# Kernel tuning notes

Hardware: AMD Instinct MI355X
Metric: run time of the kernel (lower is better)

The kernel has to match this reference:

```python
import jax, jax.numpy as jnp
import numpy as np

TOPK = 2
ROUTED_SCALING_FACTOR = 1.0


def setup_inputs() -> dict:
    key = jax.random.key(0)
    k1, k2 = jax.random.split(key)
    N, D, E = 8192, 4096, 64
    x = jax.random.normal(k1, (N, D), dtype=jnp.float32)
    expert_embeddings = jax.random.normal(k2, (E, D), dtype=jnp.float32) * 0.02
    gate_bias = jnp.zeros((E,), dtype=jnp.float32)
    return {"x": x, "expert_embeddings": expert_embeddings, "gate_bias": gate_bias}


def reference(x, expert_embeddings, gate_bias):
    # logits: (N, E) = x @ W^T, computed in fp32 as in the original
    logits = jnp.einsum('nd,ed->ne', x.astype(jnp.float32), expert_embeddings.astype(jnp.float32))
    scores = jax.nn.sigmoid(logits)
    biased_scores = scores + gate_bias  # bias only affects expert selection
    _, indices = jax.lax.top_k(biased_scores, TOPK)  # (N, topk)
    weights = jnp.take_along_axis(scores, indices, axis=-1)  # gather unbiased scores
    weights = weights / jnp.sum(weights, axis=-1, keepdims=True)
    weights = weights * ROUTED_SCALING_FACTOR
    return weights, indices, scores
```

## Files before the change

kernel.cpp:

```cpp
#include <hip/hip_runtime.h>
#include <hip/hip_bf16.h>
#include <math.h>

#define NROWS 8192
#define DDIM  4096
#define NEXP  64
#define KSPLIT 16
#define KCHUNK (DDIM / KSPLIT)
#define KSTEPS (KCHUNK / 32)

typedef __attribute__((ext_vector_type(8))) short bf16x8;
typedef __attribute__((ext_vector_type(4))) float f32x4;

__device__ inline unsigned short bf16_rne(float f) {
    unsigned u = __builtin_bit_cast(unsigned, f);
    u += 0x7FFF + ((u >> 16) & 1);
    return (unsigned short)(u >> 16);
}

__device__ inline void split8(const float* xf, bf16x8& hi, bf16x8& lo) {
#pragma unroll
    for (int j = 0; j < 8; j++) {
        const unsigned short h = bf16_rne(xf[j]);
        const float hf = __builtin_bit_cast(float, (unsigned)h << 16);
        hi[j] = (short)h;
        lo[j] = (short)bf16_rne(xf[j] - hf);
    }
}

__global__ __launch_bounds__(256) void wfrag_kernel(
    const float* __restrict__ w, unsigned short* __restrict__ whi,
    unsigned short* __restrict__ wlo, float* __restrict__ logits)
{
    const int kc = blockIdx.x;
    const int t  = threadIdx.x >> 6;
    const int l  = threadIdx.x & 63;
    const int e  = t * 16 + (l & 15);
    const int k0 = kc * 32 + ((l >> 4) * 8);
    const float* p = w + (size_t)e * DDIM + k0;
    float xf[8];
    *(float4*)&xf[0] = *(const float4*)p;
    *(float4*)&xf[4] = *(const float4*)(p + 4);
    bf16x8 hi, lo;
    split8(xf, hi, lo);
    const size_t off = ((size_t)(kc * 4 + t) * 64 + l) * 8;
    *(bf16x8*)(whi + off) = hi;
    *(bf16x8*)(wlo + off) = lo;

    const float4 z = {0.f, 0.f, 0.f, 0.f};
    float4* lz = (float4*)logits;
    const int base = (blockIdx.x * 256 + threadIdx.x) * 4;
#pragma unroll
    for (int j = 0; j < 4; j++) lz[base + j] = z;
}

__global__ __launch_bounds__(256) void gemm_partial_kernel(
    const float* __restrict__ x, const unsigned short* __restrict__ whi,
    const unsigned short* __restrict__ wlo, float* __restrict__ logits)
{
    __shared__ float ldsx[4 * 2 * 1024];

    const int tid = threadIdx.x;
    const int wv  = tid >> 6;
    const int l   = tid & 63;
    const int q   = l >> 4;
    const int col = l & 15;
    const int c7  = col & 7;
    const int r0  = blockIdx.x * 128 + wv * 32;
    const int kb  = blockIdx.y * KCHUNK;

    const int slr   = l >> 3;
    const int slotp = l & 7;

    float* ldsw = ldsx + wv * 2048;

    const unsigned short* bhp = whi + ((size_t)(kb / 32) * 4 * 64 + l) * 8;
    const unsigned short* blp = wlo + ((size_t)(kb / 32) * 4 * 64 + l) * 8;

    f32x4 acc[2][4];
#pragma unroll
    for (int m = 0; m < 2; m++)
#pragma unroll
        for (int t = 0; t < 4; t++) acc[m][t] = f32x4{0, 0, 0, 0};

    auto STAGE = [&](int buf, int s) {
#pragma unroll
        for (int g = 0; g < 4; g++) {
            const int lr   = g * 8 + slr;
            const int slot = slotp ^ (lr & 7);
            const float* gp = x + (size_t)(r0 + lr) * DDIM + kb + s * 32 + slot * 4;
            __builtin_amdgcn_global_load_lds(
                (const __attribute__((address_space(1))) void*)gp,
                (__attribute__((address_space(3))) void*)(ldsw + buf * 1024 + g * 256),
                16, 0, 0);
        }
    };

    STAGE(0, 0);
    __builtin_amdgcn_sched_barrier(0);

    for (int s = 0; s < KSTEPS; s++) {
        const int buf = s & 1;

        bf16x8 bh[4], bl[4];
        const unsigned short* bhs = bhp + (size_t)s * 4 * 64 * 8;
        const unsigned short* bls = blp + (size_t)s * 4 * 64 * 8;
#pragma unroll
        for (int t = 0; t < 4; t++) {
            bh[t] = *(const bf16x8*)(bhs + (size_t)t * 64 * 8);
            bl[t] = *(const bf16x8*)(bls + (size_t)t * 64 * 8);
        }

        asm volatile("s_waitcnt vmcnt(8)" ::: "memory");
        __builtin_amdgcn_sched_barrier(0);

        float xr[2][8];
#pragma unroll
        for (int m = 0; m < 2; m++) {
            const float* rb = ldsw + buf * 1024 + (m * 16 + col) * 32;
            const int sp0 = (q * 2) ^ c7;
            *(float4*)&xr[m][0] = *(const float4*)(rb + sp0 * 4);
            *(float4*)&xr[m][4] = *(const float4*)(rb + (sp0 ^ 1) * 4);
        }

        STAGE(buf ^ 1, (s + 1) & 7);
        __builtin_amdgcn_sched_barrier(0);

        bf16x8 ah[2], al[2];
        split8(xr[0], ah[0], al[0]);
        split8(xr[1], ah[1], al[1]);
#pragma unroll
        for (int m = 0; m < 2; m++)
#pragma unroll
            for (int t = 0; t < 4; t++) {
                acc[m][t] = __builtin_amdgcn_mfma_f32_16x16x32_bf16(ah[m], bh[t], acc[m][t], 0, 0, 0);
                acc[m][t] = __builtin_amdgcn_mfma_f32_16x16x32_bf16(ah[m], bl[t], acc[m][t], 0, 0, 0);
                acc[m][t] = __builtin_amdgcn_mfma_f32_16x16x32_bf16(al[m], bh[t], acc[m][t], 0, 0, 0);
            }
    }

#pragma unroll
    for (int m = 0; m < 2; m++)
#pragma unroll
        for (int t = 0; t < 4; t++)
#pragma unroll
            for (int r = 0; r < 4; r++)
                unsafeAtomicAdd(
                    &logits[(size_t)(r0 + m * 16 + q * 4 + r) * NEXP + t * 16 + col],
                    acc[m][t][r]);
}

__global__ __launch_bounds__(256) void gate_topk_kernel(
    const float* __restrict__ logits, const float* __restrict__ bias,
    float* __restrict__ out)
{
    const int tid = threadIdx.x;
    const int e   = tid & 63;
    const int row = blockIdx.x * 4 + (tid >> 6);
    const size_t idx = (size_t)row * NEXP + e;

    const float be    = bias[e];
    const float logit = logits[idx];
    const float score = 1.0f / (1.0f + expf(-logit));
    out[(size_t)4 * NROWS + idx] = score;

    const float biased = score + be;

    float v = biased; int bi = e;
#pragma unroll
    for (int off = 32; off; off >>= 1) {
        const float ov = __shfl_xor(v, off);
        const int   oi = __shfl_xor(bi, off);
        if (ov > v || (ov == v && oi < bi)) { v = ov; bi = oi; }
    }
    const int i1 = bi;

    float v2 = (e == i1) ? -INFINITY : biased;
    int bi2 = e;
#pragma unroll
    for (int off = 32; off; off >>= 1) {
        const float ov = __shfl_xor(v2, off);
        const int   oi = __shfl_xor(bi2, off);
        if (ov > v2 || (ov == v2 && oi < bi2)) { v2 = ov; bi2 = oi; }
    }
    const int i2 = bi2;

    const float s1 = __shfl(score, i1);
    const float s2 = __shfl(score, i2);
    if (e == 0) {
        const float inv = 1.0f / (s1 + s2);
        out[(size_t)row * 2 + 0] = s1 * inv;
        out[(size_t)row * 2 + 1] = s2 * inv;
        out[(size_t)2 * NROWS + row * 2 + 0] = (float)i1;
        out[(size_t)2 * NROWS + row * 2 + 1] = (float)i2;
    }
}

extern "C" void kernel_launch(void* const* d_in, const int* in_sizes, int n_in,
                              void* d_out, int out_size, void* d_ws, size_t ws_size,
                              hipStream_t stream)
{
    const float* x    = (const float*)d_in[0];
    const float* w    = (const float*)d_in[1];
    const float* bias = (const float*)d_in[2];
    float* out  = (float*)d_out;

    float* logits = (float*)d_ws;
    const size_t logits_bytes = (size_t)NROWS * NEXP * 4;
    unsigned short* whi = (unsigned short*)((char*)d_ws + logits_bytes);
    unsigned short* wlo = whi + (size_t)NEXP * DDIM;

    wfrag_kernel<<<DDIM / 32, 256, 0, stream>>>(w, whi, wlo, logits);
    dim3 g1(NROWS / 128, KSPLIT);
    gemm_partial_kernel<<<g1, 256, 0, stream>>>(x, whi, wlo, logits);
    gate_topk_kernel<<<NROWS / 4, 256, 0, stream>>>(logits, bias, out);
}
```

Baseline: 213.7 us.

## Triple-buffer x tiles in LDS and double-buffer W fragments in registers

Changes the split-K GEMM main loop from a two-slot LDS pipeline to a three-slot ring for the x tiles, with the async loads issued three steps ahead. The bf16 hi/lo W fragments are now loaded one step ahead into a register double buffer. Waitcnt values are adjusted to the new load order, and the loop is fully unrolled. The aim is to hide more global-load latency in this latency-bound loop, at the cost of 50% more LDS per block and more registers, which may lower occupancy.

After: 220.9 us. 1.03x slower.

```diff
diff --git a/kernel.cpp b/kernel.cpp
--- a/kernel.cpp
+++ b/kernel.cpp
@@ -58,7 +58,7 @@
     const float* __restrict__ x, const unsigned short* __restrict__ whi,
     const unsigned short* __restrict__ wlo, float* __restrict__ logits)
 {
-    __shared__ float ldsx[4 * 2 * 1024];
+    __shared__ float ldsx[4 * 3 * 1024];
 
     const int tid = threadIdx.x;
     const int wv  = tid >> 6;
@@ -72,7 +72,7 @@
     const int slr   = l >> 3;
     const int slotp = l & 7;
 
-    float* ldsw = ldsx + wv * 2048;
+    float* ldsw = ldsx + wv * 3072;
 
     const unsigned short* bhp = whi + ((size_t)(kb / 32) * 4 * 64 + l) * 8;
     const unsigned short* blp = wlo + ((size_t)(kb / 32) * 4 * 64 + l) * 8;
@@ -83,7 +83,9 @@
 #pragma unroll
         for (int t = 0; t < 4; t++) acc[m][t] = f32x4{0, 0, 0, 0};
 
-    auto STAGE = [&](int buf, int s) {
+    bf16x8 bh[2][4], bl[2][4];
+
+    auto STAGE = [&](int bufi, int s) {
 #pragma unroll
         for (int g = 0; g < 4; g++) {
             const int lr   = g * 8 + slr;
@@ -91,51 +93,61 @@
             const float* gp = x + (size_t)(r0 + lr) * DDIM + kb + s * 32 + slot * 4;
             __builtin_amdgcn_global_load_lds(
                 (const __attribute__((address_space(1))) void*)gp,
-                (__attribute__((address_space(3))) void*)(ldsw + buf * 1024 + g * 256),
+                (__attribute__((address_space(3))) void*)(ldsw + bufi * 1024 + g * 256),
                 16, 0, 0);
         }
     };
 
-    STAGE(0, 0);
-    __builtin_amdgcn_sched_barrier(0);
-
-    for (int s = 0; s < KSTEPS; s++) {
-        const int buf = s & 1;
-
-        bf16x8 bh[4], bl[4];
+    auto LOADB = [&](int rb, int s) {
         const unsigned short* bhs = bhp + (size_t)s * 4 * 64 * 8;
         const unsigned short* bls = blp + (size_t)s * 4 * 64 * 8;
 #pragma unroll
         for (int t = 0; t < 4; t++) {
-            bh[t] = *(const bf16x8*)(bhs + (size_t)t * 64 * 8);
-            bl[t] = *(const bf16x8*)(bls + (size_t)t * 64 * 8);
+            bh[rb][t] = *(const bf16x8*)(bhs + (size_t)t * 64 * 8);
+            bl[rb][t] = *(const bf16x8*)(bls + (size_t)t * 64 * 8);
         }
-
-        asm volatile("s_waitcnt vmcnt(8)" ::: "memory");
+    };
+
+    LOADB(0, 0);
+    STAGE(0, 0);
+    STAGE(1, 1);
+    STAGE(2, 2);
+    __builtin_amdgcn_sched_barrier(0);
+
+#pragma unroll
+    for (int s = 0; s < KSTEPS; s++) {
+        const int rb = s & 1;
+
+        if (s == 0) asm volatile("s_waitcnt vmcnt(8)" ::: "memory");
+        else        asm volatile("s_waitcnt vmcnt(4)" ::: "memory");
         __builtin_amdgcn_sched_barrier(0);
 
+        LOADB(rb ^ 1, (s + 1) & 7);
+        __builtin_amdgcn_sched_barrier(0);
+
         float xr[2][8];
 #pragma unroll
         for (int m = 0; m < 2; m++) {
-            const float* rb = ldsw + buf * 1024 + (m * 16 + col) * 32;
+            const float* rbp = ldsw + (s % 3) * 1024 + (m * 16 + col) * 32;
             const int sp0 = (q * 2) ^ c7;
-            *(float4*)&xr[m][0] = *(const float4*)(rb + sp0 * 4);
-            *(float4*)&xr[m][4] = *(const float4*)(rb + (sp0 ^ 1) * 4);
+            *(float4*)&xr[m][0] = *(const float4*)(rbp + sp0 * 4);
+            *(float4*)&xr[m][4] = *(const float4*)(rbp + (sp0 ^ 1) * 4);
         }
-
-        STAGE(buf ^ 1, (s + 1) & 7);
-        __builtin_amdgcn_sched_barrier(0);
 
         bf16x8 ah[2], al[2];
         split8(xr[0], ah[0], al[0]);
         split8(xr[1], ah[1], al[1]);
+
+        STAGE(s % 3, (s + 3) & 7);
+        __builtin_amdgcn_sched_barrier(0);
+
 #pragma unroll
         for (int m = 0; m < 2; m++)
 #pragma unroll
             for (int t = 0; t < 4; t++) {
-                acc[m][t] = __builtin_amdgcn_mfma_f32_16x16x32_bf16(ah[m], bh[t], acc[m][t], 0, 0, 0);
-                acc[m][t] = __builtin_amdgcn_mfma_f32_16x16x32_bf16(ah[m], bl[t], acc[m][t], 0, 0, 0);
-                acc[m][t] = __builtin_amdgcn_mfma_f32_16x16x32_bf16(al[m], bh[t], acc[m][t], 0, 0, 0);
+                acc[m][t] = __builtin_amdgcn_mfma_f32_16x16x32_bf16(ah[m], bh[rb][t], acc[m][t], 0, 0, 0);
+                acc[m][t] = __builtin_amdgcn_mfma_f32_16x16x32_bf16(ah[m], bl[rb][t], acc[m][t], 0, 0, 0);
+                acc[m][t] = __builtin_amdgcn_mfma_f32_16x16x32_bf16(al[m], bh[rb][t], acc[m][t], 0, 0, 0);
             }
     }
 
```

## Split K across waves in block and reduce partials in LDS instead of atomics

Applied to the files above, without the earlier changes.

Each block now covers 32 rows, and its four waves each take a different 256-wide K slice, so waves in a block share rows rather than rows being split across waves. Partial results are summed in LDS, and each of the four K-split blocks writes its own partial buffer. This replaces global float atomics and the zero-init of logits with plain stores. The top-k kernel then sums the four partials per logit. The costs are an extra LDS reduction with a __syncthreads, more workspace for the partial buffers, and four reads per logit in the gating kernel.

After: 211.8 us. No clear change (-0.9%).

```diff
diff --git a/kernel.cpp b/kernel.cpp
--- a/kernel.cpp
+++ b/kernel.cpp
@@ -5,9 +5,9 @@
 #define NROWS 8192
 #define DDIM  4096
 #define NEXP  64
-#define KSPLIT 16
+#define KSPLIT 4
 #define KCHUNK (DDIM / KSPLIT)
-#define KSTEPS (KCHUNK / 32)
+#define KSTEPS 8
 
 typedef __attribute__((ext_vector_type(8))) short bf16x8;
 typedef __attribute__((ext_vector_type(4))) float f32x4;
@@ -30,7 +30,7 @@
 
 __global__ __launch_bounds__(256) void wfrag_kernel(
     const float* __restrict__ w, unsigned short* __restrict__ whi,
-    unsigned short* __restrict__ wlo, float* __restrict__ logits)
+    unsigned short* __restrict__ wlo)
 {
     const int kc = blockIdx.x;
     const int t  = threadIdx.x >> 6;
@@ -46,17 +46,11 @@
     const size_t off = ((size_t)(kc * 4 + t) * 64 + l) * 8;
     *(bf16x8*)(whi + off) = hi;
     *(bf16x8*)(wlo + off) = lo;
-
-    const float4 z = {0.f, 0.f, 0.f, 0.f};
-    float4* lz = (float4*)logits;
-    const int base = (blockIdx.x * 256 + threadIdx.x) * 4;
-#pragma unroll
-    for (int j = 0; j < 4; j++) lz[base + j] = z;
 }
 
 __global__ __launch_bounds__(256) void gemm_partial_kernel(
     const float* __restrict__ x, const unsigned short* __restrict__ whi,
-    const unsigned short* __restrict__ wlo, float* __restrict__ logits)
+    const unsigned short* __restrict__ wlo, float* __restrict__ part)
 {
     __shared__ float ldsx[4 * 2 * 1024];
 
@@ -66,8 +60,9 @@
     const int q   = l >> 4;
     const int col = l & 15;
     const int c7  = col & 7;
-    const int r0  = blockIdx.x * 128 + wv * 32;
-    const int kb  = blockIdx.y * KCHUNK;
+    const int r0  = blockIdx.x * 32;
+    const int kh  = blockIdx.y;
+    const int kb  = kh * KCHUNK + wv * 256;
 
     const int slr   = l >> 3;
     const int slotp = l & 7;
@@ -99,6 +94,7 @@
     STAGE(0, 0);
     __builtin_amdgcn_sched_barrier(0);
 
+#pragma unroll
     for (int s = 0; s < KSTEPS; s++) {
         const int buf = s & 1;
 
@@ -117,13 +113,13 @@
         float xr[2][8];
 #pragma unroll
         for (int m = 0; m < 2; m++) {
-            const float* rb = ldsw + buf * 1024 + (m * 16 + col) * 32;
+            const float* rbp = ldsw + buf * 1024 + (m * 16 + col) * 32;
             const int sp0 = (q * 2) ^ c7;
-            *(float4*)&xr[m][0] = *(const float4*)(rb + sp0 * 4);
-            *(float4*)&xr[m][4] = *(const float4*)(rb + (sp0 ^ 1) * 4);
+            *(float4*)&xr[m][0] = *(const float4*)(rbp + sp0 * 4);
+            *(float4*)&xr[m][4] = *(const float4*)(rbp + (sp0 ^ 1) * 4);
         }
 
-        STAGE(buf ^ 1, (s + 1) & 7);
+        if (s + 1 < KSTEPS) STAGE(buf ^ 1, s + 1);
         __builtin_amdgcn_sched_barrier(0);
 
         bf16x8 ah[2], al[2];
@@ -139,19 +135,29 @@
             }
     }
 
+    asm volatile("s_waitcnt vmcnt(0)" ::: "memory");
+    __builtin_amdgcn_sched_barrier(0);
+
 #pragma unroll
     for (int m = 0; m < 2; m++)
 #pragma unroll
         for (int t = 0; t < 4; t++)
 #pragma unroll
             for (int r = 0; r < 4; r++)
-                unsafeAtomicAdd(
-                    &logits[(size_t)(r0 + m * 16 + q * 4 + r) * NEXP + t * 16 + col],
-                    acc[m][t][r]);
+                ldsx[wv * 2048 + (m * 16 + q * 4 + r) * 64 + t * 16 + col] = acc[m][t][r];
+
+    __syncthreads();
+
+    const f32x4* lp = (const f32x4*)ldsx;
+    const f32x4 s0 = lp[tid * 2]     + lp[512 + tid * 2]     + lp[1024 + tid * 2]     + lp[1536 + tid * 2];
+    const f32x4 s1 = lp[tid * 2 + 1] + lp[512 + tid * 2 + 1] + lp[1024 + tid * 2 + 1] + lp[1536 + tid * 2 + 1];
+    float* po = part + (size_t)kh * NROWS * NEXP + (size_t)r0 * NEXP + tid * 8;
+    *(f32x4*)po       = s0;
+    *(f32x4*)(po + 4) = s1;
 }
 
 __global__ __launch_bounds__(256) void gate_topk_kernel(
-    const float* __restrict__ logits, const float* __restrict__ bias,
+    const float* __restrict__ part, const float* __restrict__ bias,
     float* __restrict__ out)
 {
     const int tid = threadIdx.x;
@@ -159,8 +165,11 @@
     const int row = blockIdx.x * 4 + (tid >> 6);
     const size_t idx = (size_t)row * NEXP + e;
 
-    const float be    = bias[e];
-    const float logit = logits[idx];
+    const float be = bias[e];
+    float logit = 0.f;
+#pragma unroll
+    for (int s = 0; s < KSPLIT; s++)
+        logit += part[(size_t)s * NROWS * NEXP + idx];
     const float score = 1.0f / (1.0f + expf(-logit));
     out[(size_t)4 * NROWS + idx] = score;
 
@@ -205,13 +214,13 @@
     const float* bias = (const float*)d_in[2];
     float* out  = (float*)d_out;
 
-    float* logits = (float*)d_ws;
-    const size_t logits_bytes = (size_t)NROWS * NEXP * 4;
-    unsigned short* whi = (unsigned short*)((char*)d_ws + logits_bytes);
+    float* part = (float*)d_ws;
+    const size_t part_bytes = (size_t)KSPLIT * NROWS * NEXP * 4;
+    unsigned short* whi = (unsigned short*)((char*)d_ws + part_bytes);
     unsigned short* wlo = whi + (size_t)NEXP * DDIM;
 
-    wfrag_kernel<<<DDIM / 32, 256, 0, stream>>>(w, whi, wlo, logits);
-    dim3 g1(NROWS / 128, KSPLIT);
-    gemm_partial_kernel<<<g1, 256, 0, stream>>>(x, whi, wlo, logits);
-    gate_topk_kernel<<<NROWS / 4, 256, 0, stream>>>(logits, bias, out);
-}
+    wfrag_kernel<<<DDIM / 32, 256, 0, stream>>>(w, whi, wlo);
+    dim3 g1(NROWS / 32, KSPLIT);
+    gemm_partial_kernel<<<g1, 256, 0, stream>>>(x, whi, wlo, part);
+    gate_topk_kernel<<<NROWS / 4, 256, 0, stream>>>(part, bias, out);
+}
```
